# Performance work log

Hardware: AMD Instinct MI355X
Metric: run time of the kernel (lower is better)

The kernel has to match this reference:

```python
import jax, jax.numpy as jnp
import numpy as np

BITS = 4          # bit_type.bits
N_SHIFT = 30      # n in int_exp
X0 = -0.6931      # -ln(2)
COEF0 = 0.35815147
COEF1 = 0.96963238
COEF2 = 1.0


def setup_inputs() -> dict:
    key = jax.random.key(0)
    x = jax.random.normal(key, (1, 16, 2048, 2048), dtype=jnp.float32)
    scale = jnp.asarray(0.05, dtype=jnp.float32)  # scalar input scale (code collapses tensors via .max())
    return {"x": x, "scale": scale}


def _int_softmax(x, s):
    # x_int = x / s, shifted by row max (no floor here, matches torch)
    x_int = x / s
    x_int = x_int - jnp.max(x_int, axis=-1, keepdims=True)
    # ---- int_exp ----
    x0_int = jnp.floor(X0 / s)                       # negative scalar
    x_int = jnp.maximum(x_int, N_SHIFT * x0_int)
    q = jnp.floor(x_int / x0_int)                    # >= 0
    r = x_int - x0_int * q                           # remainder in (x0_int, 0]
    # ---- int_polynomial ----
    b_int = jnp.floor((COEF1 / COEF0) / s)
    c_int = jnp.floor((COEF2 / COEF0) / (s * s))
    z = r * (r + b_int) + c_int
    exp_int = jnp.maximum(jnp.floor(z * jnp.exp2(N_SHIFT - q)), 0.0)
    exp_sum = jnp.sum(exp_int, axis=-1, keepdims=True)
    return exp_int, exp_sum


def _log_round(v):
    # floor(log2(v)), bumped up by 1 when v - 2^big >= 2^(big-1)
    big = jnp.floor(jnp.log2(v))
    bump = (v - jnp.exp2(big)) >= jnp.exp2(big - 1.0)
    return jnp.where(bump, big + 1.0, big)


def reference(x, scale):
    exp_int, exp_sum = _int_softmax(x, scale)
    softmax_out = jnp.round(exp_sum / exp_int)       # inverse-softmax integer (inf where exp_int==0)
    qlog = jnp.clip(_log_round(softmax_out), 0.0, 2.0 ** BITS - 1.0)
    deq = jnp.exp2(-qlog)                            # log2-quantized softmax
    return deq / jnp.sum(deq, axis=-1, keepdims=True)
```

## Files before the change

kernel.cpp:

```cpp
#include <hip/hip_runtime.h>
#include <math.h>

#define ROWLEN 2048
#define NTHREADS 256

__global__ __launch_bounds__(NTHREADS) void qis_kernel(
    const float* __restrict__ x, const float* __restrict__ scale,
    float* __restrict__ out) {
  const int row = blockIdx.x;
  const long long base = (long long)row * ROWLEN;
  const int t = threadIdx.x;
  const int wave = t >> 6;

  __shared__ float smax[4];
  __shared__ float ssum[4];
  __shared__ float sdq[4];
  __shared__ float e2t[62];

  if (t < 62) {
    const int k = t - 15;
    const double kd = (double)k;
    const double LN2F = 0.693147182464599609375;
    const double C1   = 0.693359375;
    const double C2m  = (double)2.12194440e-4f;
    const float  a  = (float)(kd * LN2F);
    const double f1 = (double)a - kd * C1;
    const float  r  = (float)(f1 + kd * C2m);
    const double rd = (double)r;
    const float  p  = (float)(1.0 + (rd + 0.5 * rd * rd));
    e2t[t] = (float)ldexp((double)p, k);
  }

  const float s    = scale[0];
  const float rs   = __fdiv_rn(1.0f, s);
  const float x0i  = floorf(__fmul_rn(-0.6931f, rs));
  const float bint = floorf(__fmul_rn((float)(0.96963238 / 0.35815147), rs));
  const float ss   = __fmul_rn(s, s);
  const float rss  = __fdiv_rn(1.0f, ss);
  const float cint = floorf(__fmul_rn((float)(1.0 / 0.35815147), rss));
  const float lo   = __fmul_rn(30.0f, x0i);
  const float rx0  = __fdiv_rn(1.0f, x0i);

  float4 va = *(const float4*)(x + base + 8 * t);
  float4 vb = *(const float4*)(x + base + 8 * t + 4);
  float xs[8];
  {
    float xf[8] = {va.x, va.y, va.z, va.w, vb.x, vb.y, vb.z, vb.w};
#pragma unroll
    for (int j = 0; j < 8; j++) xs[j] = __fmul_rn(xf[j], rs);
  }

  float m = xs[0];
#pragma unroll
  for (int j = 1; j < 8; j++) m = fmaxf(m, xs[j]);
#pragma unroll
  for (int o = 32; o > 0; o >>= 1) m = fmaxf(m, __shfl_xor(m, o, 64));
  if ((t & 63) == 0) smax[wave] = m;
  __syncthreads();
  m = fmaxf(fmaxf(smax[0], smax[1]), fmaxf(smax[2], smax[3]));

  float ei[8];
  float pe = 0.0f;
#pragma unroll
  for (int j = 0; j < 8; j++) {
    float xi = __fsub_rn(xs[j], m);
    xi = fmaxf(xi, lo);
    float qf = floorf(__fmul_rn(xi, rx0));
    float r  = __fsub_rn(xi, __fmul_rn(x0i, qf));
    float z  = __fadd_rn(__fmul_rn(r, __fadd_rn(r, bint)), cint);
    int   qi = (int)qf;
    float e  = floorf(__fmul_rn(z, e2t[45 - qi]));
    ei[j] = fmaxf(e, 0.0f);
    pe = __fadd_rn(pe, ei[j]);
  }
#pragma unroll
  for (int o = 32; o > 0; o >>= 1)
    pe = __fadd_rn(pe, __shfl_xor(pe, o, 64));
  if ((t & 63) == 0) ssum[wave] = pe;
  __syncthreads();
  const float esum = __fadd_rn(__fadd_rn(ssum[0], ssum[1]),
                               __fadd_rn(ssum[2], ssum[3]));

  float dq[8];
  float pd = 0.0f;
#pragma unroll
  for (int j = 0; j < 8; j++) {
    float R = __fdiv_rn(esum, ei[j]);
    float v = rintf(R);
    unsigned ui = __float_as_uint(v);
    int big = (int)(ui >> 23) - 127;
    if (big > 46) big = 46;
    int bump = (__fsub_rn(v, e2t[big + 15]) >= e2t[big + 14]) ? 1 : 0;
    int q = big + bump;
    if (q > 15) q = 15;
    dq[j] = e2t[15 - q];
    pd += dq[j];
  }
#pragma unroll
  for (int o = 32; o > 0; o >>= 1) pd += __shfl_xor(pd, o, 64);
  if ((t & 63) == 0) sdq[wave] = pd;
  __syncthreads();
  const float dsum = (sdq[0] + sdq[1]) + (sdq[2] + sdq[3]);
  const float dinv = __fdiv_rn(1.0f, dsum);

  float o0[8];
#pragma unroll
  for (int j = 0; j < 8; j++) o0[j] = __fmul_rn(dq[j], dinv);
  *(float4*)(out + base + 8 * t)     = make_float4(o0[0], o0[1], o0[2], o0[3]);
  *(float4*)(out + base + 8 * t + 4) = make_float4(o0[4], o0[5], o0[6], o0[7]);
}

extern "C" void kernel_launch(void* const* d_in, const int* in_sizes, int n_in,
                              void* d_out, int out_size, void* d_ws, size_t ws_size,
                              hipStream_t stream) {
  const float* x = (const float*)d_in[0];
  const float* scale = (const float*)d_in[1];
  float* out = (float*)d_out;
  const int rows = out_size / ROWLEN;
  qis_kernel<<<dim3(rows), dim3(NTHREADS), 0, stream>>>(x, scale, out);
}
```

Baseline: 103.7 us.

## Process four rows per block to amortize setup and barriers

Each 256-thread block now handles four rows instead of one. All four rows are loaded up front and their reductions are batched, so each barrier and the per-block table and constant setup are shared across four rows. This adds memory-level parallelism per thread and cuts the grid to a quarter of its size. In exchange it raises register pressure from keeping 32 floats per thread and lowers the number of blocks available to spread across CUs.

```diff
diff --git a/kernel.cpp b/kernel.cpp
--- a/kernel.cpp
+++ b/kernel.cpp
@@ -7,14 +7,12 @@
 __global__ __launch_bounds__(NTHREADS) void qis_kernel(
     const float* __restrict__ x, const float* __restrict__ scale,
     float* __restrict__ out) {
-  const int row = blockIdx.x;
-  const long long base = (long long)row * ROWLEN;
   const int t = threadIdx.x;
   const int wave = t >> 6;
 
-  __shared__ float smax[4];
-  __shared__ float ssum[4];
-  __shared__ float sdq[4];
+  __shared__ float smax[4][4];
+  __shared__ float ssum[4][4];
+  __shared__ float sdq[4][4];
   __shared__ float e2t[62];
 
   if (t < 62) {
@@ -41,73 +39,112 @@
   const float lo   = __fmul_rn(30.0f, x0i);
   const float rx0  = __fdiv_rn(1.0f, x0i);
 
-  float4 va = *(const float4*)(x + base + 8 * t);
-  float4 vb = *(const float4*)(x + base + 8 * t + 4);
-  float xs[8];
-  {
-    float xf[8] = {va.x, va.y, va.z, va.w, vb.x, vb.y, vb.z, vb.w};
+  const long long base0 = ((long long)blockIdx.x * 4) * ROWLEN;
+
+  float a[4][8];
 #pragma unroll
-    for (int j = 0; j < 8; j++) xs[j] = __fmul_rn(xf[j], rs);
+  for (int k = 0; k < 4; k++) {
+    const float* p = x + base0 + (long long)k * ROWLEN + 8 * t;
+    float4 va = *(const float4*)(p);
+    float4 vb = *(const float4*)(p + 4);
+    a[k][0] = __fmul_rn(va.x, rs); a[k][1] = __fmul_rn(va.y, rs);
+    a[k][2] = __fmul_rn(va.z, rs); a[k][3] = __fmul_rn(va.w, rs);
+    a[k][4] = __fmul_rn(vb.x, rs); a[k][5] = __fmul_rn(vb.y, rs);
+    a[k][6] = __fmul_rn(vb.z, rs); a[k][7] = __fmul_rn(vb.w, rs);
   }
 
-  float m = xs[0];
+  float mk[4];
 #pragma unroll
-  for (int j = 1; j < 8; j++) m = fmaxf(m, xs[j]);
+  for (int k = 0; k < 4; k++) {
+    float m = a[k][0];
 #pragma unroll
-  for (int o = 32; o > 0; o >>= 1) m = fmaxf(m, __shfl_xor(m, o, 64));
-  if ((t & 63) == 0) smax[wave] = m;
+    for (int j = 1; j < 8; j++) m = fmaxf(m, a[k][j]);
+#pragma unroll
+    for (int o = 32; o > 0; o >>= 1) m = fmaxf(m, __shfl_xor(m, o, 64));
+    mk[k] = m;
+  }
+  if ((t & 63) == 0) {
+#pragma unroll
+    for (int k = 0; k < 4; k++) smax[k][wave] = mk[k];
+  }
   __syncthreads();
-  m = fmaxf(fmaxf(smax[0], smax[1]), fmaxf(smax[2], smax[3]));
+#pragma unroll
+  for (int k = 0; k < 4; k++)
+    mk[k] = fmaxf(fmaxf(smax[k][0], smax[k][1]),
+                  fmaxf(smax[k][2], smax[k][3]));
 
-  float ei[8];
-  float pe = 0.0f;
+  float pe[4];
 #pragma unroll
-  for (int j = 0; j < 8; j++) {
-    float xi = __fsub_rn(xs[j], m);
-    xi = fmaxf(xi, lo);
-    float qf = floorf(__fmul_rn(xi, rx0));
-    float r  = __fsub_rn(xi, __fmul_rn(x0i, qf));
-    float z  = __fadd_rn(__fmul_rn(r, __fadd_rn(r, bint)), cint);
-    int   qi = (int)qf;
-    float e  = floorf(__fmul_rn(z, e2t[45 - qi]));
-    ei[j] = fmaxf(e, 0.0f);
-    pe = __fadd_rn(pe, ei[j]);
+  for (int k = 0; k < 4; k++) {
+    pe[k] = 0.0f;
+#pragma unroll
+    for (int j = 0; j < 8; j++) {
+      float xi = __fsub_rn(a[k][j], mk[k]);
+      xi = fmaxf(xi, lo);
+      float qf = floorf(__fmul_rn(xi, rx0));
+      float r  = __fsub_rn(xi, __fmul_rn(x0i, qf));
+      float z  = __fadd_rn(__fmul_rn(r, __fadd_rn(r, bint)), cint);
+      int   qi = (int)qf;
+      float e  = floorf(__fmul_rn(z, e2t[45 - qi]));
+      e = fmaxf(e, 0.0f);
+      a[k][j] = e;
+      pe[k] = __fadd_rn(pe[k], e);
+    }
+#pragma unroll
+    for (int o = 32; o > 0; o >>= 1)
+      pe[k] = __fadd_rn(pe[k], __shfl_xor(pe[k], o, 64));
   }
+  if ((t & 63) == 0) {
 #pragma unroll
-  for (int o = 32; o > 0; o >>= 1)
-    pe = __fadd_rn(pe, __shfl_xor(pe, o, 64));
-  if ((t & 63) == 0) ssum[wave] = pe;
+    for (int k = 0; k < 4; k++) ssum[k][wave] = pe[k];
+  }
   __syncthreads();
-  const float esum = __fadd_rn(__fadd_rn(ssum[0], ssum[1]),
-                               __fadd_rn(ssum[2], ssum[3]));
+  float esum[4];
+#pragma unroll
+  for (int k = 0; k < 4; k++)
+    esum[k] = __fadd_rn(__fadd_rn(ssum[k][0], ssum[k][1]),
+                        __fadd_rn(ssum[k][2], ssum[k][3]));
 
-  float dq[8];
-  float pd = 0.0f;
+  float pd[4];
 #pragma unroll
-  for (int j = 0; j < 8; j++) {
-    float R = __fdiv_rn(esum, ei[j]);
-    float v = rintf(R);
-    unsigned ui = __float_as_uint(v);
-    int big = (int)(ui >> 23) - 127;
-    if (big > 46) big = 46;
-    int bump = (__fsub_rn(v, e2t[big + 15]) >= e2t[big + 14]) ? 1 : 0;
-    int q = big + bump;
-    if (q > 15) q = 15;
-    dq[j] = e2t[15 - q];
-    pd += dq[j];
+  for (int k = 0; k < 4; k++) {
+    pd[k] = 0.0f;
+#pragma unroll
+    for (int j = 0; j < 8; j++) {
+      float R = __fdiv_rn(esum[k], a[k][j]);
+      float v = rintf(R);
+      unsigned ui = __float_as_uint(v);
+      int big = (int)(ui >> 23) - 127;
+      if (big > 46) big = 46;
+      int bump = (__fsub_rn(v, e2t[big + 15]) >= e2t[big + 14]) ? 1 : 0;
+      int q = big + bump;
+      if (q > 15) q = 15;
+      float d = e2t[15 - q];
+      a[k][j] = d;
+      pd[k] += d;
+    }
+#pragma unroll
+    for (int o = 32; o > 0; o >>= 1)
+      pd[k] += __shfl_xor(pd[k], o, 64);
   }
+  if ((t & 63) == 0) {
 #pragma unroll
-  for (int o = 32; o > 0; o >>= 1) pd += __shfl_xor(pd, o, 64);
-  if ((t & 63) == 0) sdq[wave] = pd;
+    for (int k = 0; k < 4; k++) sdq[k][wave] = pd[k];
+  }
   __syncthreads();
-  const float dsum = (sdq[0] + sdq[1]) + (sdq[2] + sdq[3]);
-  const float dinv = __fdiv_rn(1.0f, dsum);
-
-  float o0[8];
 #pragma unroll
-  for (int j = 0; j < 8; j++) o0[j] = __fmul_rn(dq[j], dinv);
-  *(float4*)(out + base + 8 * t)     = make_float4(o0[0], o0[1], o0[2], o0[3]);
-  *(float4*)(out + base + 8 * t + 4) = make_float4(o0[4], o0[5], o0[6], o0[7]);
+  for (int k = 0; k < 4; k++) {
+    const float dsum = (sdq[k][0] + sdq[k][1]) + (sdq[k][2] + sdq[k][3]);
+    const float dinv = __fdiv_rn(1.0f, dsum);
+    float4 w0, w1;
+    w0.x = __fmul_rn(a[k][0], dinv); w0.y = __fmul_rn(a[k][1], dinv);
+    w0.z = __fmul_rn(a[k][2], dinv); w0.w = __fmul_rn(a[k][3], dinv);
+    w1.x = __fmul_rn(a[k][4], dinv); w1.y = __fmul_rn(a[k][5], dinv);
+    w1.z = __fmul_rn(a[k][6], dinv); w1.w = __fmul_rn(a[k][7], dinv);
+    float* p = out + base0 + (long long)k * ROWLEN + 8 * t;
+    *(float4*)(p) = w0;
+    *(float4*)(p + 4) = w1;
+  }
 }
 
 extern "C" void kernel_launch(void* const* d_in, const int* in_sizes, int n_in,
@@ -117,5 +154,5 @@
   const float* scale = (const float*)d_in[1];
   float* out = (float*)d_out;
   const int rows = out_size / ROWLEN;
-  qis_kernel<<<dim3(rows), dim3(NTHREADS), 0, stream>>>(x, scale, out);
+  qis_kernel<<<dim3(rows / 4), dim3(NTHREADS), 0, stream>>>(x, scale, out);
 }
```

New measurement: 106.9 us. +3.1%, slower.
